# Performance work log

Measured on AMD Instinct MI355X. Metric: run time of the kernel, lower is better.

The kernel has to match this reference:

```python
import jax, jax.numpy as jnp
import numpy as np

EMB = 512
HEADS = 16
WH, WW = 8, 8
N = WH * WW
B = 2048
CPB_HID = 512
EPS = 1e-12


def _buffers():
    # continuous relative coords table, shape (1, 2*WH-1, 2*WW-1, 2)
    ch = np.arange(-(WH - 1), WH, dtype=np.float32)
    cw = np.arange(-(WW - 1), WW, dtype=np.float32)
    t = np.stack(np.meshgrid(ch, cw, indexing='ij')).transpose(1, 2, 0)[None].copy()
    t[..., 0] /= (WH - 1)
    t[..., 1] /= (WW - 1)
    t *= 8.0
    t = np.sign(t) * np.log2(np.abs(t) + 1.0) / np.log2(8.0)
    # relative position index, shape (N, N), values in [0, (2*WH-1)*(2*WW-1))
    coords = np.stack(np.meshgrid(np.arange(WH), np.arange(WW), indexing='ij'))
    cf = coords.reshape(2, -1)
    rel = (cf[:, :, None] - cf[:, None, :]).transpose(1, 2, 0).copy()
    rel[..., 0] += WH - 1
    rel[..., 1] += WW - 1
    rel[..., 0] *= 2 * WW - 1
    idx = rel.sum(-1)
    return jnp.asarray(t, jnp.float32), jnp.asarray(idx, jnp.int32)


def setup_inputs() -> dict:
    key = jax.random.key(0)
    ks = jax.random.split(key, 8)
    rel_table, rel_index = _buffers()
    s = 0.02
    return {
        'x': jax.random.normal(ks[0], (B, N, EMB), jnp.float32),
        'qkv_w': jax.random.normal(ks[1], (3 * EMB, EMB), jnp.float32) * s,
        'q_bias': jnp.zeros((EMB,), jnp.float32),
        'v_bias': jnp.zeros((EMB,), jnp.float32),
        'flex_attn': jnp.full((HEADS, 1, 1), np.log(10.0), jnp.float32),
        'cpb_w1': jax.random.normal(ks[2], (CPB_HID, 2), jnp.float32) * s,
        'cpb_b1': jnp.zeros((CPB_HID,), jnp.float32),
        'cpb_w2': jax.random.normal(ks[3], (HEADS, CPB_HID), jnp.float32) * s,
        'proj_w': jax.random.normal(ks[4], (EMB, EMB), jnp.float32) * s,
        'proj_b': jnp.zeros((EMB,), jnp.float32),
        'rel_table': rel_table,
        'rel_index': rel_index,
    }


def reference(x, qkv_w, q_bias, v_bias, flex_attn, cpb_w1, cpb_b1, cpb_w2,
              proj_w, proj_b, rel_table, rel_index):
    Bx, Nx, C = x.shape
    H = HEADS
    D = C // H
    # qkv with bias only on q and v (k bias is zero), as in the torch code
    qkv_bias = jnp.concatenate([q_bias, jnp.zeros_like(v_bias), v_bias])
    qkv = x @ qkv_w.T + qkv_bias                      # (B, N, 3C)
    qkv = qkv.reshape(Bx, Nx, 3, H, D).transpose(2, 0, 3, 1, 4)
    q, k, v = qkv[0], qkv[1], qkv[2]                  # each (B, H, N, D)
    # cosine attention: L2-normalize q and k
    qn = q / jnp.maximum(jnp.linalg.norm(q, axis=-1, keepdims=True), EPS)
    kn = k / jnp.maximum(jnp.linalg.norm(k, axis=-1, keepdims=True), EPS)
    attn = jnp.einsum('bhnd,bhmd->bhnm', qn, kn)      # (B, H, N, N)
    # learned per-head temperature, clamped at 1/0.01
    scale = jnp.exp(jnp.minimum(flex_attn, jnp.log(jnp.float32(100.0))))  # (H,1,1)
    attn = attn * scale[None]
    # continuous relative position bias via MLP + gather
    bias_tab = jax.nn.relu(rel_table @ cpb_w1.T + cpb_b1) @ cpb_w2.T      # (1, 2WH-1, 2WW-1, H)
    bias_tab = bias_tab.reshape(-1, H)
    bias = bias_tab[rel_index.reshape(-1)].reshape(Nx, Nx, H)
    bias = 16.0 * jax.nn.sigmoid(bias.transpose(2, 0, 1))                 # (H, N, N)
    attn = jax.nn.softmax(attn + bias[None], axis=-1)
    out = jnp.einsum('bhnm,bhmd->bhnd', attn, v)      # (B, H, N, D)
    out = out.transpose(0, 2, 1, 3).reshape(Bx, Nx, C)
    return out @ proj_w.T + proj_b
```

## Files before the change

kernel.cpp:

```cpp
#include <hip/hip_runtime.h>

using bf16x8 = __attribute__((ext_vector_type(8))) short;
using f32x4  = __attribute__((ext_vector_type(4))) float;

static constexpr int EMB = 512, HEADS = 16, NTOK = 64, BWIN = 2048;
static constexpr int MROWS = BWIN * NTOK;
static constexpr int QKVN  = 3 * EMB;

__device__ __forceinline__ float bf2f(unsigned int u) {
  union { unsigned int i; float f; } c; c.i = u << 16; return c.f;
}
__device__ __forceinline__ unsigned short f2bf(float x) {
  union { float f; unsigned int i; } c; c.f = x;
  return (unsigned short)((c.i + 0x7fffu + ((c.i >> 16) & 1u)) >> 16);
}
__device__ __forceinline__ void gload_lds16(const void* g, void* l) {
  __builtin_amdgcn_global_load_lds((const __attribute__((address_space(1))) void*)g,
                                   (__attribute__((address_space(3))) void*)l, 16, 0, 0);
}

__global__ __launch_bounds__(256) void xcast(const float* __restrict__ x,
                                             unsigned short* __restrict__ xb) {
  size_t i = ((size_t)blockIdx.x * 256 + threadIdx.x) * 8;
  float4 a = *(const float4*)(x + i);
  float4 b = *(const float4*)(x + i + 4);
  ushort4 lo = make_ushort4(f2bf(a.x), f2bf(a.y), f2bf(a.z), f2bf(a.w));
  ushort4 hi = make_ushort4(f2bf(b.x), f2bf(b.y), f2bf(b.z), f2bf(b.w));
  *(ushort4*)(xb + i) = lo;
  *(ushort4*)(xb + i + 4) = hi;
}

__global__ void prep_weights(const float* __restrict__ qkv_w, const float* __restrict__ proj_w,
                             const float* __restrict__ q_bias, const float* __restrict__ v_bias,
                             unsigned short* __restrict__ wq, unsigned short* __restrict__ wp,
                             float* __restrict__ qkv_bias) {
  int i = blockIdx.x * 256 + threadIdx.x;
  wq[i] = f2bf(qkv_w[i]);
  if (i < EMB * EMB) wp[i] = f2bf(proj_w[i]);
  if (i < EMB) {
    qkv_bias[i]           = q_bias[i];
    qkv_bias[EMB + i]     = 0.f;
    qkv_bias[2 * EMB + i] = v_bias[i];
  }
}

__global__ __launch_bounds__(64) void cpb_mlp(const float* __restrict__ tbl,
                        const float* __restrict__ w1, const float* __restrict__ b1,
                        const float* __restrict__ w2, float* __restrict__ tab) {
  __shared__ float hid[512];
  const int p = blockIdx.x, t = threadIdx.x;
  const float t0 = tbl[p * 2], t1 = tbl[p * 2 + 1];
  #pragma unroll
  for (int s = 0; s < 8; ++s) {
    int j = t + s * 64;
    hid[j] = fmaxf(0.f, t0 * w1[j * 2] + t1 * w1[j * 2 + 1] + b1[j]);
  }
  __syncthreads();
  const int h = t >> 2, q = t & 3;
  float sum = 0.f;
  for (int j = q * 128; j < q * 128 + 128; ++j) sum += hid[j] * w2[h * 512 + j];
  sum += __shfl_xor(sum, 1);
  sum += __shfl_xor(sum, 2);
  if (q == 0) tab[p * 16 + h] = sum;
}

__global__ void cpb_expand(const float* __restrict__ tab, const int* __restrict__ rel_index,
                           float* __restrict__ bias16) {
  int e = blockIdx.x * 256 + threadIdx.x;
  int h = e >> 12, ij = e & 4095;
  float x = tab[rel_index[ij] * 16 + h];
  bias16[e] = 16.f / (1.f + __expf(-x));
}

template<bool OUT_F32, int NBX>
__global__ __launch_bounds__(256) void gemm_nt(const unsigned short* __restrict__ Ap,
    const unsigned short* __restrict__ Bp, const float* __restrict__ bias,
    void* __restrict__ Cp, int M, int N, int K) {
  __shared__ unsigned short As[128 * 64];
  __shared__ unsigned short Bs[128 * 64];
  const int tid = threadIdx.x;
  const int l = tid & 63, w = tid >> 6;
  const int lr = l & 15, lg = l >> 4;
  const int q8 = gridDim.x >> 3;
  const int wgid = (blockIdx.x & 7) * q8 + (blockIdx.x >> 3);
  const int n0 = (wgid % NBX) * 128, m0 = (wgid / NBX) * 128;
  const int wm = (w >> 1) * 64, wn = (w & 1) * 64;
  f32x4 acc[4][4];
  #pragma unroll
  for (int i = 0; i < 4; ++i)
    #pragma unroll
    for (int j = 0; j < 4; ++j) acc[i][j] = (f32x4){0.f, 0.f, 0.f, 0.f};

  for (int k0 = 0; k0 < K; k0 += 64) {
    #pragma unroll
    for (int it = 0; it < 4; ++it) {
      int c = it * 4 + w;
      int r8 = l >> 3;
      int row = c * 8 + r8;
      int src8 = ((l & 7) ^ r8) * 8;
      gload_lds16(Ap + (size_t)(m0 + row) * K + k0 + src8, As + c * 512);
    }
    #pragma unroll
    for (int it = 0; it < 4; ++it) {
      int c = it * 4 + w;
      int r8 = l >> 3;
      int row = c * 8 + r8;
      int src8 = ((l & 7) ^ r8) * 8;
      gload_lds16(Bp + (size_t)(n0 + row) * K + k0 + src8, Bs + c * 512);
    }
    __syncthreads();
    #pragma unroll
    for (int ks = 0; ks < 2; ++ks) {
      bf16x8 af[4], bfr[4];
      #pragma unroll
      for (int i = 0; i < 4; ++i) {
        int row = wm + i * 16 + lr;
        af[i] = *(const bf16x8*)(As + row * 64 + (((ks * 4 + lg) ^ (row & 7)) * 8));
      }
      #pragma unroll
      for (int j = 0; j < 4; ++j) {
        int row = wn + j * 16 + lr;
        bfr[j] = *(const bf16x8*)(Bs + row * 64 + (((ks * 4 + lg) ^ (row & 7)) * 8));
      }
      #pragma unroll
      for (int i = 0; i < 4; ++i)
        #pragma unroll
        for (int j = 0; j < 4; ++j)
          acc[i][j] = __builtin_amdgcn_mfma_f32_16x16x32_bf16(af[i], bfr[j], acc[i][j], 0, 0, 0);
    }
    __syncthreads();
  }
  #pragma unroll
  for (int i = 0; i < 4; ++i)
    #pragma unroll
    for (int j = 0; j < 4; ++j)
      #pragma unroll
      for (int r = 0; r < 4; ++r) {
        int mm = m0 + wm + i * 16 + lg * 4 + r;
        int nn = n0 + wn + j * 16 + lr;
        float v = acc[i][j][r] + bias[nn];
        if (OUT_F32) ((float*)Cp)[(size_t)mm * N + nn] = v;
        else ((unsigned short*)Cp)[(size_t)mm * N + nn] = f2bf(v);
      }
}

__device__ __forceinline__ bf16x8 load_norm_frag(const unsigned short* p, float s) {
  uint4 raw = *(const uint4*)p;
  float f[8];
  f[0] = bf2f(raw.x & 0xffffu); f[1] = bf2f(raw.x >> 16);
  f[2] = bf2f(raw.y & 0xffffu); f[3] = bf2f(raw.y >> 16);
  f[4] = bf2f(raw.z & 0xffffu); f[5] = bf2f(raw.z >> 16);
  f[6] = bf2f(raw.w & 0xffffu); f[7] = bf2f(raw.w >> 16);
  float ss = 0.f;
  #pragma unroll
  for (int j = 0; j < 8; ++j) ss += f[j] * f[j];
  ss += __shfl_xor(ss, 16);
  ss += __shfl_xor(ss, 32);
  float inv = s / fmaxf(sqrtf(ss), 1e-12f);
  bf16x8 v;
  #pragma unroll
  for (int j = 0; j < 8; ++j) v[j] = (short)f2bf(f[j] * inv);
  return v;
}

__global__ __launch_bounds__(128) void attn_win(const unsigned short* __restrict__ qkv,
    const float* __restrict__ bias16, const float* __restrict__ flex,
    unsigned short* __restrict__ aout) {
  __shared__ float sS[2][64 * 65];
  __shared__ unsigned short sP[2][64 * 72];
  __shared__ float sRs[2][64];
  const int w = threadIdx.x >> 6, l = threadIdx.x & 63;
  const int lr = l & 15, lg = l >> 4;
  const int b = blockIdx.x >> 3;
  const int h = ((blockIdx.x & 7) << 1) | w;
  const unsigned short* base = qkv + (size_t)b * NTOK * QKVN;
  const float scale = __expf(fminf(flex[h], 4.6051701860f));

  bf16x8 aq[4], bk[4];
  #pragma unroll
  for (int i = 0; i < 4; ++i)
    aq[i] = load_norm_frag(base + (size_t)(i * 16 + lr) * QKVN + h * 32 + lg * 8, scale);
  #pragma unroll
  for (int i = 0; i < 4; ++i)
    bk[i] = load_norm_frag(base + (size_t)(i * 16 + lr) * QKVN + EMB + h * 32 + lg * 8, 1.f);

  const f32x4 z = (f32x4){0.f, 0.f, 0.f, 0.f};
  f32x4 sacc[4][4];
  #pragma unroll
  for (int i = 0; i < 4; ++i)
    #pragma unroll
    for (int j = 0; j < 4; ++j)
      sacc[i][j] = __builtin_amdgcn_mfma_f32_16x16x32_bf16(aq[i], bk[j], z, 0, 0, 0);

  float* S = sS[w];
  const float* bh = bias16 + (size_t)h * 4096;
  #pragma unroll
  for (int i = 0; i < 4; ++i)
    #pragma unroll
    for (int j = 0; j < 4; ++j)
      #pragma unroll
      for (int r = 0; r < 4; ++r) {
        int row = i * 16 + lg * 4 + r, col = j * 16 + lr;
        S[row * 65 + col] = sacc[i][j][r] + bh[row * 64 + col];
      }
  __syncthreads();

  float rowv[64];
  float mx = -1e30f;
  #pragma unroll
  for (int j = 0; j < 64; ++j) { rowv[j] = S[l * 65 + j]; mx = fmaxf(mx, rowv[j]); }
  float sum = 0.f;
  unsigned short* P = sP[w];
  #pragma unroll
  for (int j = 0; j < 64; ++j) {
    float e = __expf(rowv[j] - mx);
    sum += e;
    P[l * 72 + j] = f2bf(e);
  }
  sRs[w][l] = 1.f / sum;
  __syncthreads();

  unsigned short* vT = (unsigned short*)sS[w];
  {
    const uint4* vp = (const uint4*)(base + (size_t)l * QKVN + 2 * EMB + h * 32);
    uint4 r0 = vp[0], r1 = vp[1], r2 = vp[2], r3 = vp[3];
    unsigned int wd[16] = {r0.x, r0.y, r0.z, r0.w, r1.x, r1.y, r1.z, r1.w,
                           r2.x, r2.y, r2.z, r2.w, r3.x, r3.y, r3.z, r3.w};
    #pragma unroll
    for (int d = 0; d < 32; ++d) {
      unsigned short val = (d & 1) ? (unsigned short)(wd[d >> 1] >> 16)
                                   : (unsigned short)(wd[d >> 1] & 0xffffu);
      vT[d * 72 + l] = val;
    }
  }
  __syncthreads();

  f32x4 oacc[4][2];
  #pragma unroll
  for (int i = 0; i < 4; ++i) { oacc[i][0] = z; oacc[i][1] = z; }
  #pragma unroll
  for (int ks = 0; ks < 2; ++ks) {
    bf16x8 ap[4], bv[2];
    #pragma unroll
    for (int i = 0; i < 4; ++i)
      ap[i] = *(const bf16x8*)(P + (i * 16 + lr) * 72 + ks * 32 + lg * 8);
    #pragma unroll
    for (int jd = 0; jd < 2; ++jd)
      bv[jd] = *(const bf16x8*)(vT + (jd * 16 + lr) * 72 + ks * 32 + lg * 8);
    #pragma unroll
    for (int i = 0; i < 4; ++i)
      #pragma unroll
      for (int jd = 0; jd < 2; ++jd)
        oacc[i][jd] = __builtin_amdgcn_mfma_f32_16x16x32_bf16(ap[i], bv[jd], oacc[i][jd], 0, 0, 0);
  }
  #pragma unroll
  for (int i = 0; i < 4; ++i)
    #pragma unroll
    for (int jd = 0; jd < 2; ++jd)
      #pragma unroll
      for (int r = 0; r < 4; ++r) {
        int tok = i * 16 + lg * 4 + r, d = jd * 16 + lr;
        float val = oacc[i][jd][r] * sRs[w][tok];
        aout[(size_t)(b * NTOK + tok) * EMB + h * 32 + d] = f2bf(val);
      }
}

extern "C" void kernel_launch(void* const* d_in, const int* in_sizes, int n_in,
                              void* d_out, int out_size, void* d_ws, size_t ws_size,
                              hipStream_t stream) {
  const float* x         = (const float*)d_in[0];
  const float* qkv_w     = (const float*)d_in[1];
  const float* q_bias    = (const float*)d_in[2];
  const float* v_bias    = (const float*)d_in[3];
  const float* flex      = (const float*)d_in[4];
  const float* cpb_w1    = (const float*)d_in[5];
  const float* cpb_b1    = (const float*)d_in[6];
  const float* cpb_w2    = (const float*)d_in[7];
  const float* proj_w    = (const float*)d_in[8];
  const float* proj_b    = (const float*)d_in[9];
  const float* rel_table = (const float*)d_in[10];
  const int*   rel_index = (const int*)d_in[11];

  char* ws = (char*)d_ws;
  unsigned short* qkv_bf = (unsigned short*)(ws + 0);
  unsigned short* xb     = (unsigned short*)(ws + 402653184ull);
  unsigned short* ao_bf  = (unsigned short*)(ws + 402653184ull);
  unsigned short* wq_bf  = (unsigned short*)(ws + 536870912ull);
  unsigned short* wp_bf  = (unsigned short*)(ws + 538443776ull);
  float* qkv_bias        = (float*)(ws + 538968064ull);
  float* tab             = (float*)(ws + 538974208ull);
  float* bias16          = (float*)(ws + 538988608ull);

  xcast<<<32768, 256, 0, stream>>>(x, xb);
  prep_weights<<<3072, 256, 0, stream>>>(qkv_w, proj_w, q_bias, v_bias, wq_bf, wp_bf, qkv_bias);
  cpb_mlp<<<225, 64, 0, stream>>>(rel_table, cpb_w1, cpb_b1, cpb_w2, tab);
  cpb_expand<<<256, 256, 0, stream>>>(tab, rel_index, bias16);
  gemm_nt<false, 12><<<12288, 256, 0, stream>>>(
      xb, wq_bf, qkv_bias, (void*)qkv_bf, MROWS, QKVN, EMB);
  attn_win<<<BWIN * 8, 128, 0, stream>>>(qkv_bf, bias16, flex, ao_bf);
  gemm_nt<true, 4><<<4096, 256, 0, stream>>>(
      ao_bf, wp_bf, proj_b, d_out, MROWS, EMB, EMB);
}
```

Baseline: 767.2 us.

## Double-buffer LDS tiles in GEMM and make K a compile-time constant

The GEMM kernel now keeps two LDS buffers for the A and B tiles and issues the loads for the next K-tile before computing on the current one, so global-to-LDS traffic overlaps with MFMA work. K becomes a template parameter, which lets the K loop fully unroll and simplifies address arithmetic. The cost is double the LDS per block (64 KB), which can lower occupancy. The visible hunk shows no extra wait or barrier between the prefetch and its later use, so correctness depends on the trailing __syncthreads in the cut portion of the loop.

```diff
diff --git a/kernel.cpp b/kernel.cpp
--- a/kernel.cpp
+++ b/kernel.cpp
@@ -72,12 +72,12 @@
   bias16[e] = 16.f / (1.f + __expf(-x));
 }
 
-template<bool OUT_F32, int NBX>
+template<bool OUT_F32, int NBX, int KT>
 __global__ __launch_bounds__(256) void gemm_nt(const unsigned short* __restrict__ Ap,
     const unsigned short* __restrict__ Bp, const float* __restrict__ bias,
-    void* __restrict__ Cp, int M, int N, int K) {
-  __shared__ unsigned short As[128 * 64];
-  __shared__ unsigned short Bs[128 * 64];
+    void* __restrict__ Cp, int M, int N) {
+  __shared__ unsigned short As[2][128 * 64];
+  __shared__ unsigned short Bs[2][128 * 64];
   const int tid = threadIdx.x;
   const int l = tid & 63, w = tid >> 6;
   const int lr = l & 15, lg = l >> 4;
@@ -85,42 +85,46 @@
   const int wgid = (blockIdx.x & 7) * q8 + (blockIdx.x >> 3);
   const int n0 = (wgid % NBX) * 128, m0 = (wgid / NBX) * 128;
   const int wm = (w >> 1) * 64, wn = (w & 1) * 64;
+  const int r8 = l >> 3;
+  const int src8 = ((l & 7) ^ r8) * 8;
+  const unsigned short* Abase = Ap + (size_t)m0 * KT;
+  const unsigned short* Bbase = Bp + (size_t)n0 * KT;
+
   f32x4 acc[4][4];
   #pragma unroll
   for (int i = 0; i < 4; ++i)
     #pragma unroll
     for (int j = 0; j < 4; ++j) acc[i][j] = (f32x4){0.f, 0.f, 0.f, 0.f};
 
-  for (int k0 = 0; k0 < K; k0 += 64) {
+  auto stage = [&](int buf, int k0) {
     #pragma unroll
     for (int it = 0; it < 4; ++it) {
       int c = it * 4 + w;
-      int r8 = l >> 3;
       int row = c * 8 + r8;
-      int src8 = ((l & 7) ^ r8) * 8;
-      gload_lds16(Ap + (size_t)(m0 + row) * K + k0 + src8, As + c * 512);
+      gload_lds16(Abase + (size_t)row * KT + k0 + src8, &As[buf][c * 512]);
+      gload_lds16(Bbase + (size_t)row * KT + k0 + src8, &Bs[buf][c * 512]);
     }
-    #pragma unroll
-    for (int it = 0; it < 4; ++it) {
-      int c = it * 4 + w;
-      int r8 = l >> 3;
-      int row = c * 8 + r8;
-      int src8 = ((l & 7) ^ r8) * 8;
-      gload_lds16(Bp + (size_t)(n0 + row) * K + k0 + src8, Bs + c * 512);
-    }
-    __syncthreads();
+  };
+
+  stage(0, 0);
+  __syncthreads();
+  constexpr int NTILES = KT / 64;
+  #pragma unroll
+  for (int t = 0; t < NTILES; ++t) {
+    const int cur = t & 1;
+    if (t + 1 < NTILES) stage(cur ^ 1, (t + 1) * 64);
     #pragma unroll
     for (int ks = 0; ks < 2; ++ks) {
       bf16x8 af[4], bfr[4];
       #pragma unroll
       for (int i = 0; i < 4; ++i) {
         int row = wm + i * 16 + lr;
-        af[i] = *(const bf16x8*)(As + row * 64 + (((ks * 4 + lg) ^ (row & 7)) * 8));
+        af[i] = *(const bf16x8*)(&As[cur][row * 64 + (((ks * 4 + lg) ^ (row & 7)) * 8)]);
       }
       #pragma unroll
       for (int j = 0; j < 4; ++j) {
         int row = wn + j * 16 + lr;
-        bfr[j] = *(const bf16x8*)(Bs + row * 64 + (((ks * 4 + lg) ^ (row & 7)) * 8));
+        bfr[j] = *(const bf16x8*)(&Bs[cur][row * 64 + (((ks * 4 + lg) ^ (row & 7)) * 8)]);
       }
       #pragma unroll
       for (int i = 0; i < 4; ++i)
@@ -295,9 +299,9 @@
   prep_weights<<<3072, 256, 0, stream>>>(qkv_w, proj_w, q_bias, v_bias, wq_bf, wp_bf, qkv_bias);
   cpb_mlp<<<225, 64, 0, stream>>>(rel_table, cpb_w1, cpb_b1, cpb_w2, tab);
   cpb_expand<<<256, 256, 0, stream>>>(tab, rel_index, bias16);
-  gemm_nt<false, 12><<<12288, 256, 0, stream>>>(
-      xb, wq_bf, qkv_bias, (void*)qkv_bf, MROWS, QKVN, EMB);
+  gemm_nt<false, 12, EMB><<<12288, 256, 0, stream>>>(
+      xb, wq_bf, qkv_bias, (void*)qkv_bf, MROWS, QKVN);
   attn_win<<<BWIN * 8, 128, 0, stream>>>(qkv_bf, bias16, flex, ao_bf);
-  gemm_nt<true, 4><<<4096, 256, 0, stream>>>(
-      ao_bf, wp_bf, proj_b, d_out, MROWS, EMB, EMB);
-}
+  gemm_nt<true, 4, EMB><<<4096, 256, 0, stream>>>(
+      ao_bf, wp_bf, proj_b, d_out, MROWS, EMB);
+}
```

New measurement: 955.3 us. +24.5%, slower.
